# Optimization experiments

Measured on AMD Instinct MI355X. Metric: run time of the kernel, lower is better.

The kernel has to match this reference:

```python
import jax, jax.numpy as jnp
import numpy as np

D_MODEL = 1024
D_KV = 64
N_HEADS = 16
INNER = N_HEADS * D_KV
EPS = 1e-6


def setup_inputs() -> dict:
    key = jax.random.key(0)
    ks = jax.random.split(key, 8)
    B, SQ, SKV = 2, 2048, 4096
    hidden_states = jax.random.normal(ks[0], (B, SQ, D_MODEL), dtype=jnp.float32)
    key_value_states = jax.random.normal(ks[1], (B, SKV, D_MODEL), dtype=jnp.float32)
    attention_mask = jnp.zeros((B, 1, 1, SKV), dtype=jnp.float32)
    # nn.Linear(in, out, bias=False): y = x @ W.T; store W as [in, out] here
    s = 0.02
    Wq = jax.random.normal(ks[2], (D_MODEL, INNER), dtype=jnp.float32) * s
    Wk = jax.random.normal(ks[3], (D_MODEL, INNER), dtype=jnp.float32) * s
    Wv = jax.random.normal(ks[4], (D_MODEL, INNER), dtype=jnp.float32) * s
    Wo = jax.random.normal(ks[5], (INNER, D_MODEL), dtype=jnp.float32) * s
    ln_weight = jnp.ones((D_MODEL,), dtype=jnp.float32)
    return {
        "hidden_states": hidden_states,
        "key_value_states": key_value_states,
        "attention_mask": attention_mask,
        "ln_weight": ln_weight,
        "Wq": Wq,
        "Wk": Wk,
        "Wv": Wv,
        "Wo": Wo,
    }


def _t5_rmsnorm(x, w, eps=EPS):
    # no mean subtraction, variance in fp32
    var = jnp.mean(jnp.square(x.astype(jnp.float32)), axis=-1, keepdims=True)
    return w * (x * jax.lax.rsqrt(var + eps)).astype(x.dtype)


def reference(hidden_states, key_value_states, attention_mask, ln_weight, Wq, Wk, Wv, Wo):
    B, SQ, _ = hidden_states.shape
    SKV = key_value_states.shape[1]
    normed = _t5_rmsnorm(hidden_states, ln_weight)

    # projections -> [B, H, S, Dk]
    q = (normed @ Wq).reshape(B, SQ, N_HEADS, D_KV).transpose(0, 2, 1, 3)
    k = (key_value_states @ Wk).reshape(B, SKV, N_HEADS, D_KV).transpose(0, 2, 1, 3)
    v = (key_value_states @ Wv).reshape(B, SKV, N_HEADS, D_KV).transpose(0, 2, 1, 3)

    # T5: NO 1/sqrt(d) scaling
    scores = jnp.einsum("bhqd,bhkd->bhqk", q, k) + attention_mask
    attn = jax.nn.softmax(scores.astype(jnp.float32), axis=-1).astype(scores.dtype)
    ctx = jnp.einsum("bhqk,bhkd->bhqd", attn, v)
    ctx = ctx.transpose(0, 2, 1, 3).reshape(B, SQ, INNER)
    attn_out = ctx @ Wo
    return hidden_states + attn_out
```

## Files before the change

kernel.cpp:

```cpp
#include <hip/hip_runtime.h>

typedef unsigned short u16;
typedef unsigned int u32;
typedef __attribute__((ext_vector_type(4))) float f32x4;
typedef __attribute__((ext_vector_type(8))) short short8;
typedef __attribute__((ext_vector_type(4))) short short4v;

#define BB   2
#define SQL  2048
#define SKVL 4096
#define DM   1024
#define NH   16
#define DK   64
#define L2E  1.44269504f

#if __has_builtin(__builtin_amdgcn_exp2f)
#define EXP2(x) __builtin_amdgcn_exp2f(x)
#else
#define EXP2(x) exp2f(x)
#endif

#define MFMA32(a, b, c) __builtin_amdgcn_mfma_f32_16x16x32_bf16(a, b, c, 0, 0, 0)
#define MFMA16(a, b, c) __builtin_amdgcn_mfma_f32_16x16x16bf16_1k(a, b, c, 0, 0, 0)

__device__ __forceinline__ u16 f2bf(float f) {
  union { float f; unsigned u; } v; v.f = f;
  unsigned r = v.u + 0x7fff + ((v.u >> 16) & 1);
  return (u16)(r >> 16);
}

__device__ __forceinline__ short4v pack4(float p0, float p1, float p2, float p3) {
  union { float f; u32 u; } a, b, c, d;
  a.f = p0; b.f = p1; c.f = p2; d.f = p3;
  union { uint2 v; short4v s; } r;
  r.v.x = ((a.u + 0x8000u) >> 16) | ((b.u + 0x8000u) & 0xffff0000u);
  r.v.y = ((c.u + 0x8000u) >> 16) | ((d.u + 0x8000u) & 0xffff0000u);
  return r.s;
}

__device__ __forceinline__ void gload16(const void* g, void* lds) {
  __builtin_amdgcn_global_load_lds(
      (const __attribute__((address_space(1))) unsigned int*)g,
      (__attribute__((address_space(3))) unsigned int*)lds, 16, 0, 0);
}

__global__ void pre_kernel(const float* __restrict__ hidden, const float* __restrict__ lnw,
                           const float* __restrict__ kvs,
                           const float* __restrict__ Wq, const float* __restrict__ Wk,
                           const float* __restrict__ Wv, const float* __restrict__ Wo,
                           u16* __restrict__ normed, u16* __restrict__ kvb,
                           u16* __restrict__ Wqt, u16* __restrict__ Wkt,
                           u16* __restrict__ Wvt, u16* __restrict__ Wot) {
  __shared__ float red[4];
  __shared__ float tile[32][33];
  int bid = blockIdx.x, t = threadIdx.x;
  if (bid < 4096) {
    int row = bid;
    float4 v = ((const float4*)(hidden + (size_t)row * DM))[t];
    float ss = v.x * v.x + v.y * v.y + v.z * v.z + v.w * v.w;
#pragma unroll
    for (int m = 32; m >= 1; m >>= 1) ss += __shfl_xor(ss, m, 64);
    int lane = t & 63, wv = t >> 6;
    if (lane == 0) red[wv] = ss;
    __syncthreads();
    float total = red[0] + red[1] + red[2] + red[3];
    float scale = rsqrtf(total * (1.0f / DM) + 1e-6f);
    float4 g = ((const float4*)lnw)[t];
    ushort4 o;
    o.x = f2bf(v.x * scale * g.x);
    o.y = f2bf(v.y * scale * g.y);
    o.z = f2bf(v.z * scale * g.z);
    o.w = f2bf(v.w * scale * g.w);
    ((ushort4*)(normed + (size_t)row * DM))[t] = o;
  } else if (bid < 12288) {
    int i = (bid - 4096) * 256 + t;
    float4 v = ((const float4*)kvs)[i];
    ushort4 o;
    o.x = f2bf(v.x); o.y = f2bf(v.y); o.z = f2bf(v.z); o.w = f2bf(v.w);
    ((ushort4*)kvb)[i] = o;
  } else {
    int g = bid - 12288;
    int z = g >> 10;
    const float* W = (z == 0) ? Wq : (z == 1) ? Wk : (z == 2) ? Wv : Wo;
    u16* Wt = (z == 0) ? Wqt : (z == 1) ? Wkt : (z == 2) ? Wvt : Wot;
    int xx = g & 31, yy = (g >> 5) & 31;
    int tx = t & 31, ty = t >> 5;
    int k0 = yy * 32, n0 = xx * 32;
#pragma unroll
    for (int i = 0; i < 4; i++)
      tile[ty + i * 8][tx] = W[(size_t)(k0 + ty + i * 8) * DM + n0 + tx];
    __syncthreads();
#pragma unroll
    for (int i = 0; i < 4; i++)
      Wt[(size_t)(n0 + ty + i * 8) * DM + k0 + tx] = f2bf(tile[tx][ty + i * 8]);
  }
}

__global__ void proj_kernel(const u16* __restrict__ normed, const u16* __restrict__ kvb,
                            const u16* __restrict__ Wqt, const u16* __restrict__ Wkt,
                            const u16* __restrict__ Wvt,
                            u16* __restrict__ Qb, u16* __restrict__ Kbf,
                            u16* __restrict__ Vtb) {
  const int K = 1024;
  __shared__ __align__(16) u16 Al[128 * 32];
  __shared__ __align__(16) u16 Bl[128 * 32];
  int tid = threadIdx.x, lane = tid & 63, w = tid >> 6;
  int l15 = lane & 15, quad = lane >> 4;
  int wy = w >> 1, wx = w & 1;

  int bid = blockIdx.x;
  int mode;
  const u16 *A, *Bt;
  int tm, tn;
  if (bid < 256) { mode = 0; A = normed; Bt = Wqt; tm = (bid & 31) * 128; tn = (bid >> 5) * 128; }
  else if (bid < 768) { mode = 1; A = kvb; Bt = Wkt; int kid = bid - 256; tm = (kid & 63) * 128; tn = (kid >> 6) * 128; }
  else { mode = 2; A = Wvt; Bt = kvb; int vid = bid - 768; tm = (vid & 7) * 128; tn = (vid >> 3) * 128; }

  f32x4 acc[4][4] = {};
  for (int k0 = 0; k0 < K; k0 += 32) {
    __syncthreads();
#pragma unroll
    for (int r = 0; r < 2; r++) {
      int mg = w * 2 + r;
      gload16(A + (size_t)(tm + mg * 16 + l15) * K + k0 + quad * 8, &Al[mg * 512]);
      gload16(Bt + (size_t)(tn + mg * 16 + l15) * K + k0 + quad * 8, &Bl[mg * 512]);
    }
    __syncthreads();
    short8 af[4], bfr[4];
#pragma unroll
    for (int i = 0; i < 4; i++) {
      af[i] = *(const short8*)&Al[((wy * 4 + i) * 64 + lane) * 8];
      bfr[i] = *(const short8*)&Bl[((wx * 4 + i) * 64 + lane) * 8];
    }
#pragma unroll
    for (int mt = 0; mt < 4; mt++)
#pragma unroll
      for (int nt = 0; nt < 4; nt++)
        acc[mt][nt] = MFMA32(af[mt], bfr[nt], acc[mt][nt]);
  }

#pragma unroll
  for (int mt = 0; mt < 4; mt++) {
    int m0 = tm + wy * 64 + mt * 16 + quad * 4;
#pragma unroll
    for (int nt = 0; nt < 4; nt++) {
      int n = tn + wx * 64 + nt * 16 + l15;
      if (mode == 0) {
#pragma unroll
        for (int r = 0; r < 4; r++)
          Qb[(size_t)(m0 + r) * 1024 + n] = f2bf(acc[mt][nt][r] * L2E);
      } else if (mode == 1) {
#pragma unroll
        for (int r = 0; r < 4; r++)
          Kbf[(size_t)(m0 + r) * 1024 + n] = f2bf(acc[mt][nt][r]);
      } else {
        int b = n >> 12, skv = n & 4095;
        int kvt = skv >> 6, kvl = skv & 63;
        int p = kvl >> 5, kth = (kvl >> 4) & 1, qd = (kvl >> 2) & 3, elo = kvl & 3;
        int e = kth * 4 + elo;
        int h = m0 >> 6, d0 = m0 & 63;
        size_t base = ((size_t)((b * NH + h) * 64 + kvt) << 12) + (size_t)(p * 4 + qd) * 512 + e;
#pragma unroll
        for (int r = 0; r < 4; r++)
          Vtb[base + (size_t)(d0 + r) * 8] = f2bf(acc[mt][nt][r]);
      }
    }
  }
}

__global__ __launch_bounds__(256, 2) void flash_kernel(
    const u16* __restrict__ Qp, const u16* __restrict__ Kp, const u16* __restrict__ Vtb,
    const float* __restrict__ mask, u16* __restrict__ ctx) {
  __shared__ __align__(16) char smem[81920];
  u16* Kbuf = (u16*)smem;
  u16* Vbuf = (u16*)(smem + 32768);
  float* mlog = (float*)(smem + 65536);
  float* Ox = (float*)smem;
  float* Ll = (float*)(smem + 32768);

  int tid = threadIdx.x, lane = tid & 63, w = tid >> 6;
  int l15 = lane & 15, quad = lane >> 4;
  int grp = w >> 1, wg = w & 1;
  int qb = blockIdx.x, bh = blockIdx.y;
  int b = bh >> 4, h = bh & 15;
  int q0 = qb * 128 + wg * 64;

  {
    const float* mrow = mask + (size_t)b * SKVL + tid * 16;
#pragma unroll
    for (int g = 0; g < 4; g++) {
      float4 mv = *(const float4*)(mrow + g * 4);
      float4 o; o.x = mv.x * L2E; o.y = mv.y * L2E; o.z = mv.z * L2E; o.w = mv.w * L2E;
      *(float4*)&mlog[tid * 16 + g * 4] = o;
    }
  }

  short8 qf[4][2];
#pragma unroll
  for (int mt = 0; mt < 4; mt++)
#pragma unroll
    for (int kf = 0; kf < 2; kf++)
      qf[mt][kf] = *(const short8*)(Qp + (size_t)(b * SQL + q0 + mt * 16 + l15) * DM +
                                    h * DK + kf * 32 + quad * 8);

  f32x4 of[4][4] = {};
  float ls[4] = {0.f, 0.f, 0.f, 0.f};

  const size_t vblob = (size_t)(b * NH + h) * 64 * 4096;

  auto stage = [&](int tileIdx, int buf) {
    int kv0 = tileIdx * 64;
    u16* Kd = Kbuf + (buf * 2 + grp) * 4096;
    u16* Vd = Vbuf + (buf * 2 + grp) * 4096;
#pragma unroll
    for (int r = 0; r < 4; r++) {
      int u = wg * 4 + r;
      int kt = u >> 1, kf = u & 1;
      gload16(Kp + (size_t)(b * SKVL + kv0 + kt * 16 + l15) * DM + h * DK + kf * 32 + quad * 8,
              &Kd[u * 512]);
      gload16(Vtb + vblob + (size_t)tileIdx * 4096 + u * 512 + lane * 8, &Vd[u * 512]);
    }
  };

  stage(grp, 0);
  for (int it = 0; it < 32; ++it) {
    __syncthreads();
    if (it + 1 < 32) stage((it + 1) * 2 + grp, (it + 1) & 1);
    int tileIdx = it * 2 + grp;
    int kv0 = tileIdx * 64;
    const u16* Kg = Kbuf + ((it & 1) * 2 + grp) * 4096;
    const u16* Vg = Vbuf + ((it & 1) * 2 + grp) * 4096;

#pragma unroll
    for (int ktp = 0; ktp < 2; ktp++) {
      short4v pa[2][4];
#pragma unroll
      for (int kth = 0; kth < 2; kth++) {
        int kt = ktp * 2 + kth;
        short8 k0 = *(const short8*)&Kg[((kt * 2 + 0) * 64 + lane) * 8];
        short8 k1 = *(const short8*)&Kg[((kt * 2 + 1) * 64 + lane) * 8];
        f32x4 ml = *(const f32x4*)&mlog[kv0 + kt * 16 + quad * 4];
#pragma unroll
        for (int mt = 0; mt < 4; mt++) {
          f32x4 st = {0.f, 0.f, 0.f, 0.f};
          st = MFMA32(k0, qf[mt][0], st);
          st = MFMA32(k1, qf[mt][1], st);
          float p0 = EXP2(st[0] + ml[0]);
          float p1 = EXP2(st[1] + ml[1]);
          float p2 = EXP2(st[2] + ml[2]);
          float p3 = EXP2(st[3] + ml[3]);
          ls[mt] += (p0 + p1) + (p2 + p3);
          pa[kth][mt] = pack4(p0, p1, p2, p3);
        }
      }
#pragma unroll
      for (int nt = 0; nt < 4; nt++) {
        short8 vv = *(const short8*)&Vg[((ktp * 4 + quad) * 64 + nt * 16 + l15) * 8];
        short4v vlo = {vv[0], vv[1], vv[2], vv[3]};
        short4v vhi = {vv[4], vv[5], vv[6], vv[7]};
#pragma unroll
        for (int mt = 0; mt < 4; mt++) {
          of[mt][nt] = MFMA16(pa[0][mt], vlo, of[mt][nt]);
          of[mt][nt] = MFMA16(pa[1][mt], vhi, of[mt][nt]);
        }
      }
    }
  }

#pragma unroll
  for (int mt = 0; mt < 4; mt++) {
    ls[mt] += __shfl_xor(ls[mt], 16, 64);
    ls[mt] += __shfl_xor(ls[mt], 32, 64);
  }

  __syncthreads();
  if (grp == 1) {
#pragma unroll
    for (int mt = 0; mt < 4; mt++) {
#pragma unroll
      for (int nt = 0; nt < 4; nt++)
#pragma unroll
        for (int r = 0; r < 4; r++)
          Ox[(wg * 64 + mt * 16 + quad * 4 + r) * 64 + nt * 16 + l15] = of[mt][nt][r];
      if (quad == 0) Ll[wg * 64 + mt * 16 + l15] = ls[mt];
    }
  }
  __syncthreads();
  if (grp == 0) {
#pragma unroll
    for (int mt = 0; mt < 4; mt++) {
      float lt = ls[mt] + Ll[wg * 64 + mt * 16 + l15];
#pragma unroll
      for (int r = 0; r < 4; r++) {
        float lqr = __shfl(lt, quad * 4 + r, 64);
        float inv = 1.0f / lqr;
        int ql = wg * 64 + mt * 16 + quad * 4 + r;
        int q = qb * 128 + ql;
#pragma unroll
        for (int nt = 0; nt < 4; nt++) {
          float ov = of[mt][nt][r] + Ox[ql * 64 + nt * 16 + l15];
          ctx[(size_t)(b * SQL + q) * DM + h * DK + nt * 16 + l15] = f2bf(ov * inv);
        }
      }
    }
  }
}

__global__ void ogemm_kernel(const u16* __restrict__ A, const u16* __restrict__ Bt,
                             float* __restrict__ C, const float* __restrict__ resid) {
  const int K = 1024;
  __shared__ __align__(16) u16 Al[128 * 32];
  __shared__ __align__(16) u16 Bl[128 * 32];
  int tid = threadIdx.x, lane = tid & 63, w = tid >> 6;
  int l15 = lane & 15, quad = lane >> 4;
  int wy = w >> 1, wx = w & 1;
  int tm = blockIdx.x * 128, tn = blockIdx.y * 128;
  f32x4 acc[4][4] = {};

  for (int k0 = 0; k0 < K; k0 += 32) {
    __syncthreads();
#pragma unroll
    for (int r = 0; r < 2; r++) {
      int mg = w * 2 + r;
      gload16(A + (size_t)(tm + mg * 16 + l15) * K + k0 + quad * 8, &Al[mg * 512]);
      gload16(Bt + (size_t)(tn + mg * 16 + l15) * K + k0 + quad * 8, &Bl[mg * 512]);
    }
    __syncthreads();
    short8 af[4], bfr[4];
#pragma unroll
    for (int i = 0; i < 4; i++) {
      af[i] = *(const short8*)&Al[((wy * 4 + i) * 64 + lane) * 8];
      bfr[i] = *(const short8*)&Bl[((wx * 4 + i) * 64 + lane) * 8];
    }
#pragma unroll
    for (int mt = 0; mt < 4; mt++)
#pragma unroll
      for (int nt = 0; nt < 4; nt++)
        acc[mt][nt] = MFMA32(af[mt], bfr[nt], acc[mt][nt]);
  }

#pragma unroll
  for (int mt = 0; mt < 4; mt++) {
    int m0 = tm + wy * 64 + mt * 16 + quad * 4;
#pragma unroll
    for (int nt = 0; nt < 4; nt++) {
      int n = tn + wx * 64 + nt * 16 + l15;
#pragma unroll
      for (int r = 0; r < 4; r++) {
        size_t idx = (size_t)(m0 + r) * 1024 + n;
        C[idx] = resid[idx] + acc[mt][nt][r];
      }
    }
  }
}

extern "C" void kernel_launch(void* const* d_in, const int* in_sizes, int n_in,
                              void* d_out, int out_size, void* d_ws, size_t ws_size,
                              hipStream_t stream) {
  const float* hidden = (const float*)d_in[0];
  const float* kvs    = (const float*)d_in[1];
  const float* mask   = (const float*)d_in[2];
  const float* lnw    = (const float*)d_in[3];
  const float* Wq     = (const float*)d_in[4];
  const float* Wk     = (const float*)d_in[5];
  const float* Wv     = (const float*)d_in[6];
  const float* Wo     = (const float*)d_in[7];
  char* ws = (char*)d_ws;

  u16* normed = (u16*)(ws + 0);
  u16* kvb    = (u16*)(ws + 8388608);
  u16* Wqt    = (u16*)(ws + 25165824);
  u16* Wkt    = (u16*)(ws + 27262976);
  u16* Wvt    = (u16*)(ws + 29360128);
  u16* Wot    = (u16*)(ws + 31457280);
  u16* Qb     = (u16*)(ws + 33554432);
  u16* Kbf    = (u16*)(ws + 41943040);
  u16* Vtb    = (u16*)(ws + 58720256);
  u16* ctxb   = (u16*)(ws + 75497472);

  pre_kernel<<<16384, 256, 0, stream>>>(hidden, lnw, kvs, Wq, Wk, Wv, Wo,
                                        normed, kvb, Wqt, Wkt, Wvt, Wot);
  proj_kernel<<<1280, 256, 0, stream>>>(normed, kvb, Wqt, Wkt, Wvt, Qb, Kbf, Vtb);
  flash_kernel<<<dim3(SQL / 128, BB * NH), 256, 0, stream>>>(Qb, Kbf, Vtb, mask, ctxb);
  ogemm_kernel<<<dim3(32, 8), 256, 0, stream>>>(ctxb, Wot, (float*)d_out, hidden);
}
```

Before: 330.0 us.

## Fold mask into MFMA accumulator, compute row sums via MFMA, shrink LDS

The flash kernel now seeds the score MFMA accumulator with the log2-scaled mask, loaded straight from global memory into registers and prefetched one tile ahead. This replaces the LDS mask table and the per-element adds. Row sums of the softmax numerators are computed by an MFMA against a ones vector, which removes the scalar add chains and the final cross-lane shuffles. The bf16 pack uses a v_perm byte select, and LDS drops to 64KB, which may raise occupancy. The cost is extra MFMA work and extra registers for the prefetched mask, and the row sums now come from bf16-rounded probabilities.

New measurement: 322.9 us. -2.1%, faster.

```diff
diff --git a/kernel.cpp b/kernel.cpp
--- a/kernel.cpp
+++ b/kernel.cpp
@@ -33,8 +33,8 @@
   union { float f; u32 u; } a, b, c, d;
   a.f = p0; b.f = p1; c.f = p2; d.f = p3;
   union { uint2 v; short4v s; } r;
-  r.v.x = ((a.u + 0x8000u) >> 16) | ((b.u + 0x8000u) & 0xffff0000u);
-  r.v.y = ((c.u + 0x8000u) >> 16) | ((d.u + 0x8000u) & 0xffff0000u);
+  r.v.x = __builtin_amdgcn_perm(b.u + 0x8000u, a.u + 0x8000u, 0x07060302);
+  r.v.y = __builtin_amdgcn_perm(d.u + 0x8000u, c.u + 0x8000u, 0x07060302);
   return r.s;
 }
 
@@ -171,10 +171,9 @@
 __global__ __launch_bounds__(256, 2) void flash_kernel(
     const u16* __restrict__ Qp, const u16* __restrict__ Kp, const u16* __restrict__ Vtb,
     const float* __restrict__ mask, u16* __restrict__ ctx) {
-  __shared__ __align__(16) char smem[81920];
+  __shared__ __align__(16) char smem[65536];
   u16* Kbuf = (u16*)smem;
   u16* Vbuf = (u16*)(smem + 32768);
-  float* mlog = (float*)(smem + 65536);
   float* Ox = (float*)smem;
   float* Ll = (float*)(smem + 32768);
 
@@ -185,16 +184,6 @@
   int b = bh >> 4, h = bh & 15;
   int q0 = qb * 128 + wg * 64;
 
-  {
-    const float* mrow = mask + (size_t)b * SKVL + tid * 16;
-#pragma unroll
-    for (int g = 0; g < 4; g++) {
-      float4 mv = *(const float4*)(mrow + g * 4);
-      float4 o; o.x = mv.x * L2E; o.y = mv.y * L2E; o.z = mv.z * L2E; o.w = mv.w * L2E;
-      *(float4*)&mlog[tid * 16 + g * 4] = o;
-    }
-  }
-
   short8 qf[4][2];
 #pragma unroll
   for (int mt = 0; mt < 4; mt++)
@@ -204,9 +193,11 @@
                                     h * DK + kf * 32 + quad * 8);
 
   f32x4 of[4][4] = {};
-  float ls[4] = {0.f, 0.f, 0.f, 0.f};
+  f32x4 la[4] = {};
+  const short4v ones = {0x3F80, 0x3F80, 0x3F80, 0x3F80};
 
   const size_t vblob = (size_t)(b * NH + h) * 64 * 4096;
+  const float* mrow = mask + (size_t)b * SKVL;
 
   auto stage = [&](int tileIdx, int buf) {
     int kv0 = tileIdx * 64;
@@ -222,12 +213,24 @@
     }
   };
 
+  f32x4 mlc[4], mln[4];
+  {
+    int kv0 = grp * 64;
+#pragma unroll
+    for (int kt = 0; kt < 4; kt++)
+      mlc[kt] = *(const f32x4*)(mrow + kv0 + kt * 16 + quad * 4) * L2E;
+  }
   stage(grp, 0);
+
   for (int it = 0; it < 32; ++it) {
     __syncthreads();
-    if (it + 1 < 32) stage((it + 1) * 2 + grp, (it + 1) & 1);
-    int tileIdx = it * 2 + grp;
-    int kv0 = tileIdx * 64;
+    if (it + 1 < 32) {
+      stage((it + 1) * 2 + grp, (it + 1) & 1);
+      int kvn = ((it + 1) * 2 + grp) * 64;
+#pragma unroll
+      for (int kt = 0; kt < 4; kt++)
+        mln[kt] = *(const f32x4*)(mrow + kvn + kt * 16 + quad * 4) * L2E;
+    }
     const u16* Kg = Kbuf + ((it & 1) * 2 + grp) * 4096;
     const u16* Vg = Vbuf + ((it & 1) * 2 + grp) * 4096;
 
@@ -239,19 +242,18 @@
         int kt = ktp * 2 + kth;
         short8 k0 = *(const short8*)&Kg[((kt * 2 + 0) * 64 + lane) * 8];
         short8 k1 = *(const short8*)&Kg[((kt * 2 + 1) * 64 + lane) * 8];
-        f32x4 ml = *(const f32x4*)&mlog[kv0 + kt * 16 + quad * 4];
 #pragma unroll
         for (int mt = 0; mt < 4; mt++) {
-          f32x4 st = {0.f, 0.f, 0.f, 0.f};
+          f32x4 st = mlc[kt];
           st = MFMA32(k0, qf[mt][0], st);
           st = MFMA32(k1, qf[mt][1], st);
-          float p0 = EXP2(st[0] + ml[0]);
-          float p1 = EXP2(st[1] + ml[1]);
-          float p2 = EXP2(st[2] + ml[2]);
-          float p3 = EXP2(st[3] + ml[3]);
-          ls[mt] += (p0 + p1) + (p2 + p3);
-          pa[kth][mt] = pack4(p0, p1, p2, p3);
+          pa[kth][mt] = pack4(EXP2(st[0]), EXP2(st[1]), EXP2(st[2]), EXP2(st[3]));
         }
+      }
+#pragma unroll
+      for (int mt = 0; mt < 4; mt++) {
+        la[mt] = MFMA16(pa[0][mt], ones, la[mt]);
+        la[mt] = MFMA16(pa[1][mt], ones, la[mt]);
       }
 #pragma unroll
       for (int nt = 0; nt < 4; nt++) {
@@ -265,12 +267,8 @@
         }
       }
     }
-  }
-
-#pragma unroll
-  for (int mt = 0; mt < 4; mt++) {
-    ls[mt] += __shfl_xor(ls[mt], 16, 64);
-    ls[mt] += __shfl_xor(ls[mt], 32, 64);
+#pragma unroll
+    for (int kt = 0; kt < 4; kt++) mlc[kt] = mln[kt];
   }
 
   __syncthreads();
@@ -282,19 +280,19 @@
 #pragma unroll
         for (int r = 0; r < 4; r++)
           Ox[(wg * 64 + mt * 16 + quad * 4 + r) * 64 + nt * 16 + l15] = of[mt][nt][r];
-      if (quad == 0) Ll[wg * 64 + mt * 16 + l15] = ls[mt];
+      if (l15 == 0)
+#pragma unroll
+        for (int r = 0; r < 4; r++) Ll[wg * 64 + mt * 16 + quad * 4 + r] = la[mt][r];
     }
   }
   __syncthreads();
   if (grp == 0) {
 #pragma unroll
-    for (int mt = 0; mt < 4; mt++) {
-      float lt = ls[mt] + Ll[wg * 64 + mt * 16 + l15];
+    for (int mt = 0; mt < 4; mt++)
 #pragma unroll
       for (int r = 0; r < 4; r++) {
-        float lqr = __shfl(lt, quad * 4 + r, 64);
-        float inv = 1.0f / lqr;
         int ql = wg * 64 + mt * 16 + quad * 4 + r;
+        float inv = 1.0f / (la[mt][r] + Ll[ql]);
         int q = qb * 128 + ql;
 #pragma unroll
         for (int nt = 0; nt < 4; nt++) {
@@ -302,7 +300,6 @@
           ctx[(size_t)(b * SQL + q) * DM + h * DK + nt * 16 + l15] = f2bf(ov * inv);
         }
       }
-    }
   }
 }
 
```
